# Kernel optimization log

Hardware: AMD Instinct MI355X
Metric: run time of the kernel (lower is better)

Reference implementation:

```python
import jax, jax.numpy as jnp
import numpy as np

B, S, D, H = 4, 1024, 1024, 16
DH = D // H  # head_dim = 64


def setup_inputs() -> dict:
    key = jax.random.key(0)
    kq, kk, kv, kl, kwq, kwk, kwv, kwo = jax.random.split(key, 8)
    query = jax.random.normal(kq, (B, S, D), dtype=jnp.float32)
    key_t = jax.random.normal(kk, (B, S, D), dtype=jnp.float32)
    value = jax.random.normal(kv, (B, S, D), dtype=jnp.float32)
    # padding: keys at positions >= valid length are padded (True)
    lengths = jax.random.randint(kl, (B,), S // 2, S + 1)
    key_padding_mask = jnp.arange(S)[None, :] >= lengths[:, None]  # [B,S] bool
    scale = 1.0 / np.sqrt(D)
    Wq = jax.random.normal(kwq, (D, D), dtype=jnp.float32) * scale
    Wk = jax.random.normal(kwk, (D, D), dtype=jnp.float32) * scale
    Wv = jax.random.normal(kwv, (D, D), dtype=jnp.float32) * scale
    Wo = jax.random.normal(kwo, (D, D), dtype=jnp.float32) * scale
    gamma = jnp.ones((H,), dtype=jnp.float32)
    return {"query": query, "key": key_t, "value": value,
            "key_padding_mask": key_padding_mask,
            "Wq": Wq, "Wk": Wk, "Wv": Wv, "Wo": Wo, "gamma": gamma}


def reference(query, key, value, key_padding_mask, Wq, Wk, Wv, Wo, gamma):
    # nn.Linear(x) = x @ W.T (bias=False)
    q = jnp.einsum('bsd,ed->bse', query, Wq).reshape(B, S, H, DH).transpose(0, 2, 1, 3)  # [B,H,S,Dh]
    k = jnp.einsum('bsd,ed->bse', key, Wk).reshape(B, S, H, DH).transpose(0, 2, 1, 3)
    v = jnp.einsum('bsd,ed->bse', value, Wv).reshape(B, S, H, DH).transpose(0, 2, 1, 3)
    scores = jnp.einsum('bhqd,bhkd->bhqk', q, k) / jnp.sqrt(jnp.float32(DH))
    pad = key_padding_mask[:, None, None, :]  # [B,1,1,S]
    scores = jnp.where(pad, -jnp.inf, scores)
    v = jnp.where(key_padding_mask[:, None, :, None], 0.0, v)
    attn = jax.nn.softmax(scores, axis=-1)  # dropout p=0 (eval) -> identity
    ws = jnp.einsum('bhqk,bhkd->bhqd', attn, v)
    ws = ws * gamma[None, :, None, None]  # per-head scale
    ws = ws.transpose(0, 2, 1, 3).reshape(B, S, D)
    return jnp.einsum('bsd,ed->bse', ws, Wo)
```

## Files before the change

kernel.cpp:

```cpp
#include <hip/hip_runtime.h>
#include <math.h>

#define S_LEN 1024
#define DMODEL 1024

typedef __attribute__((ext_vector_type(8))) short bf16x8;
typedef __attribute__((ext_vector_type(4))) short bf16x4;
typedef __attribute__((ext_vector_type(4))) float f32x4;

#define MFMA16(a, b, c) __builtin_amdgcn_mfma_f32_16x16x32_bf16(a, b, c, 0, 0, 0)

#define WP (1024u * 1024u)
#define XP (4u * 1024u * 1024u)

__device__ __forceinline__ unsigned short rne_bf16(float f) {
    unsigned u = __float_as_uint(f);
    u += 0x7FFFu + ((u >> 16) & 1u);
    return (unsigned short)(u >> 16);
}

__device__ __forceinline__ void split_rne(float f, unsigned short& h, unsigned short& l) {
    unsigned short hh = rne_bf16(f);
    float lf = f - __uint_as_float(((unsigned)hh) << 16);
    h = hh;
    l = rne_bf16(lf);
}

typedef const __attribute__((address_space(1))) unsigned int* gas_t;
typedef __attribute__((address_space(3))) unsigned int* las_t;
__device__ __forceinline__ void glds16(const void* g, void* l) {
    __builtin_amdgcn_global_load_lds((gas_t)g, (las_t)l, 16, 0, 0);
}

__global__ __launch_bounds__(256)
void convert_wx(const float* __restrict__ W0, const float* __restrict__ W1,
                const float* __restrict__ W2, const float* __restrict__ W3,
                const float* __restrict__ Xq, const float* __restrict__ Xk,
                const float* __restrict__ Xv, const int* __restrict__ mask,
                unsigned short* __restrict__ Wpl, unsigned short* __restrict__ Xbase) {
    int blk = blockIdx.x;
    if (blk < 4096) {
        const int which = blk >> 10;
        const float* W = which == 0 ? W0 : which == 1 ? W1 : which == 2 ? W2 : W3;
        int i = ((blk & 1023) * 256 + threadIdx.x) * 4;
        float4 f = *(const float4*)&W[i];
        if (which == 3) {
            unsigned short* hi = Wpl + 3 * WP;
            unsigned short* lo = Wpl + 4 * WP;
            bf16x4 h, l;
            unsigned short hh, ll;
            split_rne(f.x, hh, ll); h[0] = (short)hh; l[0] = (short)ll;
            split_rne(f.y, hh, ll); h[1] = (short)hh; l[1] = (short)ll;
            split_rne(f.z, hh, ll); h[2] = (short)hh; l[2] = (short)ll;
            split_rne(f.w, hh, ll); h[3] = (short)hh; l[3] = (short)ll;
            *(bf16x4*)&hi[i] = h;
            *(bf16x4*)&lo[i] = l;
        } else {
            unsigned short* hi = Wpl + (size_t)which * WP;
            bf16x4 h;
            h[0] = (short)rne_bf16(f.x);
            h[1] = (short)rne_bf16(f.y);
            h[2] = (short)rne_bf16(f.z);
            h[3] = (short)rne_bf16(f.w);
            *(bf16x4*)&hi[i] = h;
        }
    } else {
        blk -= 4096;
        const int which = blk >> 12;
        const float* X = which == 0 ? Xq : which == 1 ? Xk : Xv;
        unsigned short* Xr = Xbase + (size_t)which * XP;
        int i = ((blk & 4095) * 256 + threadIdx.x) * 4;
        if (which != 0) {
            const int b = i >> 20, s = (i >> 10) & 1023;
            if (mask[b * 1024 + s]) {
                if (mask[b * 1024 + (s & ~127)]) return;
                bf16x4 zz = {0, 0, 0, 0};
                *(bf16x4*)&Xr[i] = zz;
                return;
            }
        }
        float4 f = *(const float4*)&X[i];
        bf16x4 h;
        h[0] = (short)rne_bf16(f.x);
        h[1] = (short)rne_bf16(f.y);
        h[2] = (short)rne_bf16(f.z);
        h[3] = (short)rne_bf16(f.w);
        *(bf16x4*)&Xr[i] = h;
    }
}

__global__ __launch_bounds__(256)
void gemm_proj(const unsigned short* __restrict__ Xbase,
               const unsigned short* __restrict__ Wpl,
               const int* __restrict__ mask,
               unsigned short* __restrict__ Obase) {
    __shared__ unsigned short AS[128 * 32];
    __shared__ unsigned short BS[128 * 32];

    const int z = blockIdx.z;
    const unsigned short* A = Xbase + (size_t)z * XP;
    const unsigned short* B = Wpl + (size_t)z * WP;

    const int t = threadIdx.x, lane = t & 63, w = t >> 6;
    const int quad = lane >> 4, l15 = lane & 15;
    const int wr = w & 1, wc = w >> 1;

    const int linb = blockIdx.x + (blockIdx.y << 3);
    const int swz = ((linb & 7) << 5) + (linb >> 3);
    const int bx = swz & 7, by = swz >> 3;
    const int rowBase = by * 128, colBase = bx * 128;

    if (z && mask[(by >> 3) * 1024 + ((by & 7) << 7)]) return;

    const unsigned short* gA[2];
    const unsigned short* gB[2];
    unsigned short* lA[2];
    unsigned short* lB[2];
    #pragma unroll
    for (int e = 0; e < 2; e++) {
        int row = w * 32 + e * 16 + (lane >> 2);
        int cg = (lane & 3) ^ ((row >> 1) & 3);
        gA[e] = A + (size_t)(rowBase + row) * 1024 + cg * 8;
        gB[e] = B + (size_t)(colBase + row) * 1024 + cg * 8;
        lA[e] = &AS[(w * 32 + e * 16) * 32];
        lB[e] = &BS[(w * 32 + e * 16) * 32];
    }

    int aAd[4], bAd[4];
    #pragma unroll
    for (int i = 0; i < 4; i++) {
        int ra = wr * 64 + i * 16 + l15;
        aAd[i] = ra * 32 + (quad ^ ((ra >> 1) & 3)) * 8;
        int rb = wc * 64 + i * 16 + l15;
        bAd[i] = rb * 32 + (quad ^ ((rb >> 1) & 3)) * 8;
    }

    f32x4 acc[4][4] = {};

    for (int kt = 0; kt < 32; kt++) {
        if (kt) __syncthreads();
        const int ko = kt * 32;
        glds16(gA[0] + ko, lA[0]);
        glds16(gA[1] + ko, lA[1]);
        glds16(gB[0] + ko, lB[0]);
        glds16(gB[1] + ko, lB[1]);
        __syncthreads();

        bf16x8 af[4], bfr[4];
        #pragma unroll
        for (int i = 0; i < 4; i++) af[i] = *(const bf16x8*)&AS[aAd[i]];
        #pragma unroll
        for (int j = 0; j < 4; j++) bfr[j] = *(const bf16x8*)&BS[bAd[j]];
        #pragma unroll
        for (int j = 0; j < 4; j++)
            #pragma unroll
            for (int i = 0; i < 4; i++)
                acc[i][j] = MFMA16(af[i], bfr[j], acc[i][j]);
    }

    unsigned short* O = Obase + (size_t)z * XP;
    #pragma unroll
    for (int i = 0; i < 4; i++)
        #pragma unroll
        for (int j = 0; j < 4; j++) {
            const int m0 = rowBase + wr * 64 + i * 16 + quad * 4;
            const int n = colBase + wc * 64 + j * 16 + l15;
            const int bb = m0 >> 10, s = m0 & 1023, hh = n >> 6, dh = n & 63;
            const size_t hb = ((size_t)(bb * 16 + hh)) << 16;
            if (z == 2) {
                bf16x4 v4;
                #pragma unroll
                for (int r = 0; r < 4; r++) v4[r] = (short)rne_bf16(acc[i][j][r]);
                *(bf16x4*)&O[hb + (size_t)dh * 1024 + s] = v4;
            } else {
                #pragma unroll
                for (int r = 0; r < 4; r++)
                    O[hb + (size_t)(s + r) * 64 + dh] = rne_bf16(acc[i][j][r]);
            }
        }
}

__global__ __launch_bounds__(256)
void gemm_out2(const unsigned short* __restrict__ A,
               const unsigned short* __restrict__ Bh, const unsigned short* __restrict__ Bl,
               float* __restrict__ Cf) {
    __shared__ unsigned short AS[128 * 32];
    __shared__ unsigned short BhS[64 * 32], BlS[64 * 32];

    const int t = threadIdx.x, lane = t & 63, w = t >> 6;
    const int quad = lane >> 4, l15 = lane & 15;
    const int wr = w & 1, wc = w >> 1;

    const int linb = blockIdx.x + (blockIdx.y << 4);
    const int swz = ((linb & 7) << 6) + (linb >> 3);
    const int bx = swz & 15, by = swz >> 4;
    const int rowBase = by * 128, colBase = bx * 64;

    const unsigned short* gA[2];
    unsigned short* lA[2];
    #pragma unroll
    for (int e = 0; e < 2; e++) {
        int row = w * 32 + e * 16 + (lane >> 2);
        int cg = (lane & 3) ^ ((row >> 1) & 3);
        gA[e] = A + (size_t)(rowBase + row) * 1024 + cg * 8;
        lA[e] = &AS[(w * 32 + e * 16) * 32];
    }
    const unsigned short *gBh, *gBl;
    unsigned short *lBh, *lBl;
    {
        int row = w * 16 + (lane >> 2);
        int cg = (lane & 3) ^ ((row >> 1) & 3);
        gBh = Bh + (size_t)(colBase + row) * 1024 + cg * 8;
        gBl = Bl + (size_t)(colBase + row) * 1024 + cg * 8;
        lBh = &BhS[(w * 16) * 32];
        lBl = &BlS[(w * 16) * 32];
    }

    int aAd[4], bAd[2];
    #pragma unroll
    for (int i = 0; i < 4; i++) {
        int ra = wr * 64 + i * 16 + l15;
        aAd[i] = ra * 32 + (quad ^ ((ra >> 1) & 3)) * 8;
    }
    #pragma unroll
    for (int j = 0; j < 2; j++) {
        int rb = wc * 32 + j * 16 + l15;
        bAd[j] = rb * 32 + (quad ^ ((rb >> 1) & 3)) * 8;
    }

    f32x4 acc[4][2] = {};

    for (int kt = 0; kt < 32; kt++) {
        if (kt) __syncthreads();
        const int ko = kt * 32;
        glds16(gA[0] + ko, lA[0]);
        glds16(gA[1] + ko, lA[1]);
        glds16(gBh + ko, lBh);
        glds16(gBl + ko, lBl);
        __syncthreads();

        bf16x8 af[4], bhf[2], blf[2];
        #pragma unroll
        for (int i = 0; i < 4; i++) af[i] = *(const bf16x8*)&AS[aAd[i]];
        #pragma unroll
        for (int j = 0; j < 2; j++) {
            bhf[j] = *(const bf16x8*)&BhS[bAd[j]];
            blf[j] = *(const bf16x8*)&BlS[bAd[j]];
        }
        #pragma unroll
        for (int j = 0; j < 2; j++)
            #pragma unroll
            for (int i = 0; i < 4; i++) {
                acc[i][j] = MFMA16(af[i], bhf[j], acc[i][j]);
                acc[i][j] = MFMA16(af[i], blf[j], acc[i][j]);
            }
    }

    #pragma unroll
    for (int i = 0; i < 4; i++)
        #pragma unroll
        for (int j = 0; j < 2; j++)
            #pragma unroll
            for (int r = 0; r < 4; r++) {
                int m = rowBase + wr * 64 + i * 16 + quad * 4 + r;
                int n = colBase + wc * 32 + j * 16 + l15;
                Cf[(size_t)m * 1024 + n] = acc[i][j][r];
            }
}

__global__ __launch_bounds__(256)
void attn_mfma(const unsigned short* __restrict__ Qr, const unsigned short* __restrict__ Kr,
               const unsigned short* __restrict__ Vt,
               const int* __restrict__ mask, const float* __restrict__ gamma,
               unsigned short* __restrict__ WSr) {
    __shared__ int maskS[1024];
    __shared__ unsigned short Ks[64 * 72];
    __shared__ unsigned short Vs[64 * 72];
    __shared__ unsigned short Ph[4 * 16 * 72];

    const int t = threadIdx.x, lane = t & 63, w = t >> 6;
    const int quad = lane >> 4, l15 = lane & 15;

    const int linb = blockIdx.x + (blockIdx.y << 4);
    const int swz = ((linb & 7) << 5) + (linb >> 3);
    const int qx = swz & 15, h = swz >> 4;

    const int q0 = qx * 64, b = blockIdx.z;
    const size_t hb = ((size_t)(b * 16 + h)) << 16;

    ((int4*)maskS)[t] = ((const int4*)(mask + b * 1024))[t];

    bf16x8 qhi[2];
    {
        const int qrow = q0 + w * 16 + l15;
        const size_t qb = hb + (size_t)qrow * 64 + quad * 8;
        qhi[0] = *(const bf16x8*)&Qr[qb];
        qhi[1] = *(const bf16x8*)&Qr[qb + 32];
    }

    const int sc = (t & 7) * 8;
    const int sr = t >> 3;

    f32x4 o[4] = {};
    float lsum[4] = {0.f, 0.f, 0.f, 0.f};

    bf16x8 kreg[2], vreg[2];
    #pragma unroll
    for (int e = 0; e < 2; e++) {
        int row = e * 32 + sr;
        kreg[e] = *(const bf16x8*)&Kr[hb + (size_t)row * 64 + sc];
        vreg[e] = *(const bf16x8*)&Vt[hb + (size_t)row * 1024 + sc];
    }
    __syncthreads();
    #pragma unroll
    for (int e = 0; e < 2; e++) {
        int row = e * 32 + sr;
        *(bf16x8*)&Ks[row * 72 + sc] = kreg[e];
        *(bf16x8*)&Vs[row * 72 + sc] = vreg[e];
    }
    __syncthreads();

    for (int jt = 0; jt < 16; jt++) {
        const int j0 = jt * 64;
        if (maskS[j0]) break;
        const bool partial = maskS[j0 + 63] != 0;
        const int j0n = j0 + 64;
        const bool pf = (jt < 15) && (maskS[j0n] == 0);

        if (pf) {
            #pragma unroll
            for (int e = 0; e < 2; e++) {
                int row = e * 32 + sr;
                kreg[e] = *(const bf16x8*)&Kr[hb + (size_t)(j0n + row) * 64 + sc];
                vreg[e] = *(const bf16x8*)&Vt[hb + (size_t)row * 1024 + j0n + sc];
            }
        }

        f32x4 s4[4] = {};
        __builtin_amdgcn_s_setprio(1);
        #pragma unroll
        for (int nj = 0; nj < 4; nj++) {
            int kr = (nj * 16 + l15) * 72 + quad * 8;
            #pragma unroll
            for (int kk = 0; kk < 2; kk++) {
                bf16x8 kv = *(const bf16x8*)&Ks[kr + kk * 32];
                s4[nj] = MFMA16(qhi[kk], kv, s4[nj]);
            }
        }
        __builtin_amdgcn_s_setprio(0);

        if (partial) {
            #pragma unroll
            for (int nj = 0; nj < 4; nj++) {
                int mk = maskS[j0 + nj * 16 + l15];
                #pragma unroll
                for (int r = 0; r < 4; r++) {
                    float p = mk ? 0.f : __expf(s4[nj][r] * 0.125f);
                    lsum[r] += p;
                    Ph[(w * 16 + quad * 4 + r) * 72 + nj * 16 + l15] = rne_bf16(p);
                }
            }
        } else {
            #pragma unroll
            for (int nj = 0; nj < 4; nj++) {
                #pragma unroll
                for (int r = 0; r < 4; r++) {
                    float p = __expf(s4[nj][r] * 0.125f);
                    lsum[r] += p;
                    Ph[(w * 16 + quad * 4 + r) * 72 + nj * 16 + l15] = rne_bf16(p);
                }
            }
        }

        bf16x8 ph[2];
        #pragma unroll
        for (int ks = 0; ks < 2; ks++)
            ph[ks] = *(const bf16x8*)&Ph[(w * 16 + l15) * 72 + ks * 32 + quad * 8];
        __builtin_amdgcn_s_setprio(1);
        #pragma unroll
        for (int dt = 0; dt < 4; dt++) {
            int vr = (dt * 16 + l15) * 72 + quad * 8;
            #pragma unroll
            for (int ks = 0; ks < 2; ks++) {
                bf16x8 vv = *(const bf16x8*)&Vs[vr + ks * 32];
                o[dt] = MFMA16(ph[ks], vv, o[dt]);
            }
        }
        __builtin_amdgcn_s_setprio(0);

        if (pf) {
            __syncthreads();
            #pragma unroll
            for (int e = 0; e < 2; e++) {
                int row = e * 32 + sr;
                *(bf16x8*)&Ks[row * 72 + sc] = kreg[e];
                *(bf16x8*)&Vs[row * 72 + sc] = vreg[e];
            }
            __syncthreads();
        }
    }

    #pragma unroll
    for (int r = 0; r < 4; r++) {
        lsum[r] += __shfl_xor(lsum[r], 1);
        lsum[r] += __shfl_xor(lsum[r], 2);
        lsum[r] += __shfl_xor(lsum[r], 4);
        lsum[r] += __shfl_xor(lsum[r], 8);
    }

    const float g = gamma[h];
    #pragma unroll
    for (int r = 0; r < 4; r++) {
        const int qrow = q0 + w * 16 + quad * 4 + r;
        const float sc2 = g / lsum[r];
        const size_t base = ((size_t)b * 1024 + qrow) * 1024 + h * 64;
        #pragma unroll
        for (int dt = 0; dt < 4; dt++)
            WSr[base + dt * 16 + l15] = rne_bf16(o[dt][r] * sc2);
    }
}

extern "C" void kernel_launch(void* const* d_in, const int* in_sizes, int n_in,
                              void* d_out, int out_size, void* d_ws, size_t ws_size,
                              hipStream_t stream) {
    const float* query = (const float*)d_in[0];
    const float* key   = (const float*)d_in[1];
    const float* value = (const float*)d_in[2];
    const int*   mask  = (const int*)d_in[3];
    const float* Wq    = (const float*)d_in[4];
    const float* Wk    = (const float*)d_in[5];
    const float* Wv    = (const float*)d_in[6];
    const float* Wo    = (const float*)d_in[7];
    const float* gamma = (const float*)d_in[8];
    float* out = (float*)d_out;

    unsigned short* u = (unsigned short*)d_ws;
    unsigned short* Xbase = u;
    unsigned short* Obase = u + 3 * XP;
    unsigned short* Wpl   = u + 6 * XP;
    unsigned short* WSr   = Xbase;
    unsigned short* Qr = Obase, *Kr = Obase + XP, *Vt = Obase + 2 * XP;
    unsigned short* Woh = Wpl + 3 * WP, *Wol = Wpl + 4 * WP;

    convert_wx<<<16384, 256, 0, stream>>>(Wq, Wk, Wv, Wo, query, key, value, mask, Wpl, Xbase);

    gemm_proj<<<dim3(8, 32, 3), 256, 0, stream>>>(Xbase, Wpl, mask, Obase);

    attn_mfma<<<dim3(16, 16, 4), 256, 0, stream>>>(Qr, Kr, Vt, mask, gamma, WSr);

    gemm_out2<<<dim3(16, 32), 256, 0, stream>>>(WSr, Woh, Wol, out);
}
```

Baseline: 202.5 us.

## Fuse fp32-to-bf16 activation conversion into projection GEMM A-tile loads

Stops converting the query/key/value activations to bf16 in a separate pass. The projection GEMM now stages fp32 A tiles directly into shared memory, using a new XOR swizzle, and converts them to bf16 with packed cvt instructions before the MFMA. This removes a full read-and-write pass over the activations and shrinks the conversion launch to weights only. In exchange, the GEMM loads twice as many bytes for A per k-step, uses more shared memory, and is re-read by each of the 8 column blocks. The masked-row zeroing that the conversion kernel used to do is gone, so padded rows now carry projections of real data into K/V.

After: 215.9 us. 6.6% more time.

```diff
diff --git a/kernel.cpp b/kernel.cpp
--- a/kernel.cpp
+++ b/kernel.cpp
@@ -26,6 +26,20 @@
     l = rne_bf16(lf);
 }
 
+__device__ __forceinline__ unsigned cvt_pk_bf16(float lo, float hi) {
+    unsigned r;
+    asm("v_cvt_pk_bf16_f32 %0, %1, %2" : "=v"(r) : "v"(lo), "v"(hi));
+    return r;
+}
+__device__ __forceinline__ bf16x8 cvt8(f32x4 lo, f32x4 hi) {
+    union { unsigned u[4]; bf16x8 v; } r;
+    r.u[0] = cvt_pk_bf16(lo[0], lo[1]);
+    r.u[1] = cvt_pk_bf16(lo[2], lo[3]);
+    r.u[2] = cvt_pk_bf16(hi[0], hi[1]);
+    r.u[3] = cvt_pk_bf16(hi[2], hi[3]);
+    return r.v;
+}
+
 typedef const __attribute__((address_space(1))) unsigned int* gas_t;
 typedef __attribute__((address_space(3))) unsigned int* las_t;
 __device__ __forceinline__ void glds16(const void* g, void* l) {
@@ -35,70 +49,45 @@
 __global__ __launch_bounds__(256)
 void convert_wx(const float* __restrict__ W0, const float* __restrict__ W1,
                 const float* __restrict__ W2, const float* __restrict__ W3,
-                const float* __restrict__ Xq, const float* __restrict__ Xk,
-                const float* __restrict__ Xv, const int* __restrict__ mask,
-                unsigned short* __restrict__ Wpl, unsigned short* __restrict__ Xbase) {
+                unsigned short* __restrict__ Wpl) {
     int blk = blockIdx.x;
-    if (blk < 4096) {
-        const int which = blk >> 10;
-        const float* W = which == 0 ? W0 : which == 1 ? W1 : which == 2 ? W2 : W3;
-        int i = ((blk & 1023) * 256 + threadIdx.x) * 4;
-        float4 f = *(const float4*)&W[i];
-        if (which == 3) {
-            unsigned short* hi = Wpl + 3 * WP;
-            unsigned short* lo = Wpl + 4 * WP;
-            bf16x4 h, l;
-            unsigned short hh, ll;
-            split_rne(f.x, hh, ll); h[0] = (short)hh; l[0] = (short)ll;
-            split_rne(f.y, hh, ll); h[1] = (short)hh; l[1] = (short)ll;
-            split_rne(f.z, hh, ll); h[2] = (short)hh; l[2] = (short)ll;
-            split_rne(f.w, hh, ll); h[3] = (short)hh; l[3] = (short)ll;
-            *(bf16x4*)&hi[i] = h;
-            *(bf16x4*)&lo[i] = l;
-        } else {
-            unsigned short* hi = Wpl + (size_t)which * WP;
-            bf16x4 h;
-            h[0] = (short)rne_bf16(f.x);
-            h[1] = (short)rne_bf16(f.y);
-            h[2] = (short)rne_bf16(f.z);
-            h[3] = (short)rne_bf16(f.w);
-            *(bf16x4*)&hi[i] = h;
-        }
+    const int which = blk >> 10;
+    const float* W = which == 0 ? W0 : which == 1 ? W1 : which == 2 ? W2 : W3;
+    int i = ((blk & 1023) * 256 + threadIdx.x) * 4;
+    float4 f = *(const float4*)&W[i];
+    if (which == 3) {
+        unsigned short* hi = Wpl + 3 * WP;
+        unsigned short* lo = Wpl + 4 * WP;
+        bf16x4 h, l;
+        unsigned short hh, ll;
+        split_rne(f.x, hh, ll); h[0] = (short)hh; l[0] = (short)ll;
+        split_rne(f.y, hh, ll); h[1] = (short)hh; l[1] = (short)ll;
+        split_rne(f.z, hh, ll); h[2] = (short)hh; l[2] = (short)ll;
+        split_rne(f.w, hh, ll); h[3] = (short)hh; l[3] = (short)ll;
+        *(bf16x4*)&hi[i] = h;
+        *(bf16x4*)&lo[i] = l;
     } else {
-        blk -= 4096;
-        const int which = blk >> 12;
-        const float* X = which == 0 ? Xq : which == 1 ? Xk : Xv;
-        unsigned short* Xr = Xbase + (size_t)which * XP;
-        int i = ((blk & 4095) * 256 + threadIdx.x) * 4;
-        if (which != 0) {
-            const int b = i >> 20, s = (i >> 10) & 1023;
-            if (mask[b * 1024 + s]) {
-                if (mask[b * 1024 + (s & ~127)]) return;
-                bf16x4 zz = {0, 0, 0, 0};
-                *(bf16x4*)&Xr[i] = zz;
-                return;
-            }
-        }
-        float4 f = *(const float4*)&X[i];
+        unsigned short* hi = Wpl + (size_t)which * WP;
         bf16x4 h;
         h[0] = (short)rne_bf16(f.x);
         h[1] = (short)rne_bf16(f.y);
         h[2] = (short)rne_bf16(f.z);
         h[3] = (short)rne_bf16(f.w);
-        *(bf16x4*)&Xr[i] = h;
+        *(bf16x4*)&hi[i] = h;
     }
 }
 
 __global__ __launch_bounds__(256)
-void gemm_proj(const unsigned short* __restrict__ Xbase,
+void gemm_proj(const float* __restrict__ Xq, const float* __restrict__ Xk,
+               const float* __restrict__ Xv,
                const unsigned short* __restrict__ Wpl,
                const int* __restrict__ mask,
                unsigned short* __restrict__ Obase) {
-    __shared__ unsigned short AS[128 * 32];
+    __shared__ float ASf[128 * 32];
     __shared__ unsigned short BS[128 * 32];
 
     const int z = blockIdx.z;
-    const unsigned short* A = Xbase + (size_t)z * XP;
+    const float* A = z == 0 ? Xq : z == 1 ? Xk : Xv;
     const unsigned short* B = Wpl + (size_t)z * WP;
 
     const int t = threadIdx.x, lane = t & 63, w = t >> 6;
@@ -112,25 +101,32 @@
 
     if (z && mask[(by >> 3) * 1024 + ((by & 7) << 7)]) return;
 
-    const unsigned short* gA[2];
+    const float* gA[4];
+    float* lAf[4];
+    #pragma unroll
+    for (int e = 0; e < 4; e++) {
+        int row = w * 32 + e * 8 + (lane >> 3);
+        int cg = (lane & 7) ^ (row & 7);
+        gA[e] = A + (size_t)(rowBase + row) * 1024 + cg * 4;
+        lAf[e] = &ASf[(w * 32 + e * 8) * 32];
+    }
     const unsigned short* gB[2];
-    unsigned short* lA[2];
     unsigned short* lB[2];
     #pragma unroll
     for (int e = 0; e < 2; e++) {
         int row = w * 32 + e * 16 + (lane >> 2);
         int cg = (lane & 3) ^ ((row >> 1) & 3);
-        gA[e] = A + (size_t)(rowBase + row) * 1024 + cg * 8;
         gB[e] = B + (size_t)(colBase + row) * 1024 + cg * 8;
-        lA[e] = &AS[(w * 32 + e * 16) * 32];
         lB[e] = &BS[(w * 32 + e * 16) * 32];
     }
 
-    int aAd[4], bAd[4];
+    int aAdf[4][2], bAd[4];
     #pragma unroll
     for (int i = 0; i < 4; i++) {
         int ra = wr * 64 + i * 16 + l15;
-        aAd[i] = ra * 32 + (quad ^ ((ra >> 1) & 3)) * 8;
+        #pragma unroll
+        for (int h2 = 0; h2 < 2; h2++)
+            aAdf[i][h2] = ra * 32 + (((2 * quad + h2) ^ (ra & 7)) << 2);
         int rb = wc * 64 + i * 16 + l15;
         bAd[i] = rb * 32 + (quad ^ ((rb >> 1) & 3)) * 8;
     }
@@ -140,15 +136,21 @@
     for (int kt = 0; kt < 32; kt++) {
         if (kt) __syncthreads();
         const int ko = kt * 32;
-        glds16(gA[0] + ko, lA[0]);
-        glds16(gA[1] + ko, lA[1]);
+        glds16(gA[0] + ko, lAf[0]);
+        glds16(gA[1] + ko, lAf[1]);
+        glds16(gA[2] + ko, lAf[2]);
+        glds16(gA[3] + ko, lAf[3]);
         glds16(gB[0] + ko, lB[0]);
         glds16(gB[1] + ko, lB[1]);
         __syncthreads();
 
         bf16x8 af[4], bfr[4];
         #pragma unroll
-        for (int i = 0; i < 4; i++) af[i] = *(const bf16x8*)&AS[aAd[i]];
+        for (int i = 0; i < 4; i++) {
+            f32x4 lo = *(const f32x4*)&ASf[aAdf[i][0]];
+            f32x4 hi = *(const f32x4*)&ASf[aAdf[i][1]];
+            af[i] = cvt8(lo, hi);
+        }
         #pragma unroll
         for (int j = 0; j < 4; j++) bfr[j] = *(const bf16x8*)&BS[bAd[j]];
         #pragma unroll
@@ -435,16 +437,15 @@
     float* out = (float*)d_out;
 
     unsigned short* u = (unsigned short*)d_ws;
-    unsigned short* Xbase = u;
-    unsigned short* Obase = u + 3 * XP;
-    unsigned short* Wpl   = u + 6 * XP;
-    unsigned short* WSr   = Xbase;
+    unsigned short* WSr   = u;
+    unsigned short* Obase = u + XP;
+    unsigned short* Wpl   = u + 4 * XP;
     unsigned short* Qr = Obase, *Kr = Obase + XP, *Vt = Obase + 2 * XP;
     unsigned short* Woh = Wpl + 3 * WP, *Wol = Wpl + 4 * WP;
 
-    convert_wx<<<16384, 256, 0, stream>>>(Wq, Wk, Wv, Wo, query, key, value, mask, Wpl, Xbase);
-
-    gemm_proj<<<dim3(8, 32, 3), 256, 0, stream>>>(Xbase, Wpl, mask, Obase);
+    convert_wx<<<4096, 256, 0, stream>>>(Wq, Wk, Wv, Wo, Wpl);
+
+    gemm_proj<<<dim3(8, 32, 3), 256, 0, stream>>>(query, key, value, Wpl, mask, Obase);
 
     attn_mfma<<<dim3(16, 16, 4), 256, 0, stream>>>(Qr, Kr, Vt, mask, gamma, WSr);
 
```
